# Kernel tuning notes

Measured on AMD Instinct MI355X. Metric: run time of the kernel, lower is better.

Reference implementation:

```python
import jax, jax.numpy as jnp
import numpy as np
from jax import lax

H = 16          # num heads
D_CONV = 4      # causal conv kernel width
NORMALIZER = 16.0
EPS = 1e-5


def _causal_conv_silu(x, w):
    # x: [B, L, D], w: [D, W] depthwise causal conv, then silu
    B, L, D = x.shape
    xp = jnp.pad(x, ((0, 0), (D_CONV - 1, 0), (0, 0)))
    y = sum(xp[:, k:k + L, :] * w[:, k] for k in range(D_CONV))
    return jax.nn.silu(y)


def _gla_scan(q, k, v, gk):
    # q,k,gk: [B,H,L,dk]; v: [B,H,L,dv]
    B, h, L, dk = q.shape
    dv = v.shape[-1]
    qT = jnp.moveaxis(q, 2, 0)
    kT = jnp.moveaxis(k, 2, 0)
    vT = jnp.moveaxis(v, 2, 0)
    gT = jnp.moveaxis(gk, 2, 0)

    def step(S, inp):
        qt, kt, vt, gt = inp  # [B,H,dk] / [B,H,dv]
        S = S * jnp.exp(gt)[..., None] + kt[..., None] * vt[..., None, :]
        ot = jnp.einsum('bhk,bhkv->bhv', qt, S)
        return S, ot

    S0 = jnp.zeros((B, h, dk, dv), q.dtype)
    S, o = lax.scan(step, S0, (qT, kT, vT, gT))
    return jnp.moveaxis(o, 0, 2), S  # [B,H,L,dv], final state


def setup_inputs() -> dict:
    key = jax.random.key(0)
    ks = jax.random.split(key, 9)
    L, B, D = 8192, 8, 1024
    s = lambda fan: 1.0 / np.sqrt(fan)
    return {
        'x': jax.random.normal(ks[0], (L, B, D), jnp.float32),
        'conv_w': jax.random.normal(ks[1], (D, D_CONV), jnp.float32) * s(D_CONV),
        'Wq': jax.random.normal(ks[2], (D, D // 2), jnp.float32) * s(D),
        'Wkg': jax.random.normal(ks[3], (D, D // 2), jnp.float32) * s(D),
        'Wv': jax.random.normal(ks[4], (D, D), jnp.float32) * s(D),
        'Wg': jax.random.normal(ks[5], (D, D), jnp.float32) * s(D),
        'bg': jax.random.normal(ks[6], (D,), jnp.float32) * 0.02,
        'Wout': jax.random.normal(ks[7], (D, D), jnp.float32) * s(D),
        'aug_balance': jnp.zeros((D // 2,), jnp.float32),
    }


def reference(x, conv_w, Wq, Wkg, Wv, Wg, bg, Wout, aug_balance):
    # x: [L, B, D] -> [B, L, D]
    xb = jnp.swapaxes(x, 0, 1)
    xb = _causal_conv_silu(xb, conv_w)

    q = xb @ Wq                      # [B,L,D/2]
    k_gate = xb @ Wkg                # [B,L,D/2]
    v = xb @ Wv                      # [B,L,D]
    g = xb @ Wg + bg                 # [B,L,D]

    gk = jax.nn.log_sigmoid(k_gate) / NORMALIZER
    k = 1.0 - jnp.exp(gk)

    B, L, _ = q.shape
    split = lambda t: t.reshape(B, L, H, -1).transpose(0, 2, 1, 3)  # b h l d
    qh, kh, gkh, vh = split(q), split(k), split(gk), split(v)
    dk = qh.shape[-1]

    # fused_chunk_gla default scale = dk ** -0.5 (applied to q internally)
    o, new_state = _gla_scan(qh * (dk ** -0.5), kh, vh, gkh)

    # meta self-augmentation (uses unscaled q)
    aug = aug_balance.reshape(H, dk)
    aug_w = jnp.einsum('bhlk,hk,bhlk->bhl', qh, aug, kh)
    o = o + jax.nn.sigmoid(aug_w[..., None] * vh)

    # group norm: LayerNorm over head_dim, no affine
    mu = o.mean(-1, keepdims=True)
    var = o.var(-1, keepdims=True)
    o = (o - mu) * lax.rsqrt(var + EPS)

    o = o.transpose(0, 2, 1, 3).reshape(B, L, -1)  # [B,L,D]
    out = (jax.nn.silu(g) * o) @ Wout
    return jnp.swapaxes(out, 0, 1), new_state  # [L,B,D], [B,H,dk,dv]
```

## Files before the change

### kernel.cpp

```cpp
#include <hip/hip_runtime.h>
#include <stdint.h>

typedef __attribute__((ext_vector_type(4))) float f32x4;
typedef _Float16 f16x8 __attribute__((ext_vector_type(8)));
typedef __attribute__((ext_vector_type(8))) unsigned short u16x8;
typedef __attribute__((ext_vector_type(2))) unsigned int u32x2;
typedef unsigned short u16;
typedef unsigned int u32;

#define LSEQ 8192
#define BB 8
#define DD 1024
#define MM 65536
#define NCH 128

__device__ __forceinline__ u16 f2h(float f) {
    _Float16 h = (_Float16)f;
    return *(u16*)&h;
}
__device__ __forceinline__ float h2f(u16 u) {
    _Float16 h = *(_Float16*)&u;
    return (float)h;
}

__device__ __forceinline__ void gload_lds16(const void* g, void* l) {
    __builtin_amdgcn_global_load_lds(
        (const __attribute__((address_space(1))) u32*)g,
        (__attribute__((address_space(3))) u32*)l, 16, 0, 0);
}

__global__ __launch_bounds__(256) void k_conv_silu(const float* __restrict__ x,
                                                   const float* __restrict__ w,
                                                   u16* __restrict__ xb) {
    int m = blockIdx.x;
    int b = m >> 13, l = m & 8191;
    int d0 = threadIdx.x * 4;
    f32x4 wv[4];
#pragma unroll
    for (int j = 0; j < 4; j++) wv[j] = *(const f32x4*)&w[(d0 + j) * 4];
    float acc[4] = {0.f, 0.f, 0.f, 0.f};
#pragma unroll
    for (int kk = 0; kk < 4; kk++) {
        int lp = l - 3 + kk;
        if (lp >= 0) {
            f32x4 xv = *(const f32x4*)&x[((size_t)(lp * BB + b)) * DD + d0];
#pragma unroll
            for (int j = 0; j < 4; j++) acc[j] += xv[j] * wv[j][kk];
        }
    }
    u16 o[4];
#pragma unroll
    for (int j = 0; j < 4; j++) {
        float a = acc[j];
        o[j] = f2h(a / (1.f + __expf(-a)));
    }
    u32x2 pk;
    pk.x = (u32)o[0] | ((u32)o[1] << 16);
    pk.y = (u32)o[2] | ((u32)o[3] << 16);
    *(u32x2*)&xb[(size_t)m * DD + d0] = pk;
}

__global__ __launch_bounds__(256) void k_packW(const float* __restrict__ Wq,
                                               const float* __restrict__ Wkg,
                                               const float* __restrict__ Wv,
                                               const float* __restrict__ Wg,
                                               const float* __restrict__ Wout,
                                               u16* __restrict__ Wcat,
                                               u16* __restrict__ WoutT) {
    int idx = blockIdx.x * 256 + threadIdx.x;
    const int T1 = 3072 * 1024;
    if (idx < T1) {
        int n = idx >> 10, kk = idx & 1023;
        float v;
        if (n < 512)        v = Wq [kk * 512 + n];
        else if (n < 1024)  v = Wkg[kk * 512 + (n - 512)];
        else if (n < 2048)  v = Wv [kk * 1024 + (n - 1024)];
        else                v = Wg [kk * 1024 + (n - 2048)];
        Wcat[idx] = f2h(v);
    } else {
        int j = idx - T1;
        if (j < 1024 * 1024) {
            int n = j >> 10, kk = j & 1023;
            WoutT[j] = f2h(Wout[kk * 1024 + n]);
        }
    }
}

template <int MODE>
__device__ __forceinline__ void epi_frag(f32x4 v, int grow0, int gcol,
                                         u16* __restrict__ qo, u16* __restrict__ gko,
                                         u16* __restrict__ ko, u16* __restrict__ vo,
                                         u16* __restrict__ sgo, const float* __restrict__ bg,
                                         float* __restrict__ out) {
#pragma unroll
    for (int rr = 0; rr < 4; rr++) {
        int grow = grow0 + rr;
        float val = v[rr];
        if (MODE == 1) {
            if (gcol < 512) {
                qo[(size_t)grow * 512 + gcol] = f2h(val);
            } else if (gcol < 1024) {
                float ls = fminf(val, 0.f) - log1pf(__expf(-fabsf(val)));
                float gkv = ls * 0.0625f;
                gko[(size_t)grow * 512 + (gcol - 512)] = f2h(gkv);
                ko [(size_t)grow * 512 + (gcol - 512)] = f2h(-expm1f(gkv));
            } else if (gcol < 2048) {
                vo[(size_t)grow * 1024 + (gcol - 1024)] = f2h(val);
            } else {
                float gg = val + bg[gcol - 2048];
                sgo[(size_t)grow * 1024 + (gcol - 2048)] = f2h(gg / (1.f + __expf(-gg)));
            }
        } else {
            int l = grow & 8191, b = grow >> 13;
            out[((size_t)(l * BB + b)) * DD + gcol] = val;
        }
    }
}

template <int MODE>
__global__ __launch_bounds__(256, 3) void k_gemm_bt(
    const u16* __restrict__ A, const u16* __restrict__ Bt, int nt_tiles,
    u16* __restrict__ qo, u16* __restrict__ gko, u16* __restrict__ ko,
    u16* __restrict__ vo, u16* __restrict__ sgo, const float* __restrict__ bg,
    float* __restrict__ out) {
    const int K = 1024;
    __shared__ __align__(16) u16 Sm[20480];
    int tid = threadIdx.x;
    int w = tid >> 6, lane = tid & 63;
    int wm = w >> 1, wn = w & 1;
    int lr = lane & 15, lk = lane >> 4;

    int xcd = blockIdx.x & 7;
    int cidx = blockIdx.x >> 3;
    int grpsz = nt_tiles * 4;
    int grp = cidx / grpsz;
    int r = cidx - grp * grpsz;
    int ntile = r >> 2;
    int mts_per_chunk = (gridDim.x >> 3) / nt_tiles;
    int mtile = xcd * mts_per_chunk + grp * 4 + (r & 3);
    int m0 = mtile << 8, n0 = ntile << 6;

#define DECL_ACC(MT) f32x4 a##MT##_0 = {0.f,0.f,0.f,0.f}, a##MT##_1 = {0.f,0.f,0.f,0.f};
    DECL_ACC(0) DECL_ACC(1) DECL_ACC(2) DECL_ACC(3)
    DECL_ACC(4) DECL_ACC(5) DECL_ACC(6) DECL_ACC(7)
#undef DECL_ACC

    int row = tid >> 2;
    int sslot = (tid & 3) ^ ((tid >> 3) & 3);
    const u16* gA = A + (size_t)(m0 + row) * K + sslot * 8;
    const u16* gB = Bt + (size_t)(n0 + row) * K + sslot * 8;
    char* lA = (char*)Sm + w * 1024;
    char* lB = (char*)Sm + 16384 + w * 1024;

#define STAGE(TT, OB) { \
    int k1 = (TT) << 5; \
    gload_lds16(gA + k1, lA + (OB)); \
    gload_lds16(gA + (size_t)64 * K + k1, lA + (OB) + 4096); \
    gload_lds16(gA + (size_t)128 * K + k1, lA + (OB) + 8192); \
    gload_lds16(gA + (size_t)192 * K + k1, lA + (OB) + 12288); \
    gload_lds16(gB + k1, lB + (OB)); }

#define MFMA_ROW(MT) { \
    f16x8 av = *(const f16x8*)&As[(wm * 128 + MT * 16 + lr) * 32 + acsl]; \
    a##MT##_0 = __builtin_amdgcn_mfma_f32_16x16x32_f16(av, b0, a##MT##_0, 0, 0, 0); \
    a##MT##_1 = __builtin_amdgcn_mfma_f32_16x16x32_f16(av, b1, a##MT##_1, 0, 0, 0); }

#define COMPUTE() { \
    int acsl = (lk ^ ((lr >> 1) & 3)) * 8; \
    f16x8 b0 = *(const f16x8*)&Bs[(wn * 32 +  0 + lr) * 32 + acsl]; \
    f16x8 b1 = *(const f16x8*)&Bs[(wn * 32 + 16 + lr) * 32 + acsl]; \
    __builtin_amdgcn_s_setprio(1); \
    MFMA_ROW(0) MFMA_ROW(1) MFMA_ROW(2) MFMA_ROW(3) \
    MFMA_ROW(4) MFMA_ROW(5) MFMA_ROW(6) MFMA_ROW(7) \
    __builtin_amdgcn_s_setprio(0); }

    STAGE(0, 0)
    STAGE(1, 20480)

    for (int t = 0; t < 31; ++t) {
        asm volatile("s_waitcnt vmcnt(5)" ::: "memory");
        __builtin_amdgcn_sched_barrier(0);
        __builtin_amdgcn_s_barrier();
        {
            const u16* As = Sm + (t & 1) * 10240;
            const u16* Bs = As + 8192;
            COMPUTE()
        }
        __builtin_amdgcn_s_barrier();
        __builtin_amdgcn_sched_barrier(0);
        if (t < 30) {
            STAGE(t + 2, (t & 1) * 20480)
        }
    }
    asm volatile("s_waitcnt vmcnt(0)" ::: "memory");
    __builtin_amdgcn_sched_barrier(0);
    __builtin_amdgcn_s_barrier();
    {
        const u16* As = Sm + 10240;
        const u16* Bs = As + 8192;
        COMPUTE()
    }
#undef COMPUTE
#undef MFMA_ROW
#undef STAGE

#define EPI_ROW(MT) { \
    int gr0 = m0 + wm * 128 + MT * 16 + lk * 4; \
    epi_frag<MODE>(a##MT##_0, gr0, n0 + wn * 32 +  0 + lr, qo, gko, ko, vo, sgo, bg, out); \
    epi_frag<MODE>(a##MT##_1, gr0, n0 + wn * 32 + 16 + lr, qo, gko, ko, vo, sgo, bg, out); }
    EPI_ROW(0) EPI_ROW(1) EPI_ROW(2) EPI_ROW(3)
    EPI_ROW(4) EPI_ROW(5) EPI_ROW(6) EPI_ROW(7)
#undef EPI_ROW
}

__global__ __launch_bounds__(64) void k_pass1(const u16* __restrict__ gkb,
                                              const u16* __restrict__ kb,
                                              const u16* __restrict__ vb,
                                              float* __restrict__ Mo,
                                              float* __restrict__ eGC) {
    __shared__ __align__(16) float kkT[64 * 32];
    int bhc = blockIdx.x;
    int c = bhc & 127, bh = bhc >> 7;
    int h = bh & 15, b = bh >> 4;
    int m0 = b * LSEQ + c * 64;
    int lane = threadIdx.x;
    if (lane < 32) {
        int i = lane;
        size_t base = (size_t)m0 * 512 + h * 32 + i;
        float G = 0.f;
        for (int t = 0; t < 64; t++) {
            G += h2f(gkb[base + (size_t)t * 512]);
            G = fmaxf(G, -60.f);
            kkT[t * 32 + i] = h2f(kb[base + (size_t)t * 512]) * __expf(-G);
        }
        eGC[bhc * 32 + i] = __expf(G);
    }
    __syncthreads();
    float Ma[32];
#pragma unroll
    for (int i = 0; i < 32; i++) Ma[i] = 0.f;
    size_t vbase = (size_t)m0 * 1024 + h * 64 + lane;
    for (int t = 0; t < 64; t++) {
        float vj = h2f(vb[vbase + (size_t)t * 1024]);
#pragma unroll
        for (int i4 = 0; i4 < 32; i4 += 4) {
            f32x4 kk4 = *(const f32x4*)&kkT[t * 32 + i4];
            Ma[i4 + 0] += kk4[0] * vj;
            Ma[i4 + 1] += kk4[1] * vj;
            Ma[i4 + 2] += kk4[2] * vj;
            Ma[i4 + 3] += kk4[3] * vj;
        }
    }
    size_t mb = (size_t)bhc * 2048 + lane;
#pragma unroll
    for (int i = 0; i < 32; i++) Mo[mb + i * 64] = Ma[i];
}

__global__ __launch_bounds__(64) void k_pass2(float* Mbuf, float* Sbuf,
                                              const float* __restrict__ eGC,
                                              float* __restrict__ state_out, int aliased) {
    int blk = blockIdx.x;
    int bh = blk >> 2, iq = blk & 3;
    int i0 = iq * 8;
    int j = threadIdx.x;
    float S[8];
#pragma unroll
    for (int i = 0; i < 8; i++) S[i] = 0.f;
    for (int c = 0; c < NCH; c++) {
        size_t base = ((size_t)bh * NCH + c) * 2048;
        float mv[8], ev[8];
#pragma unroll
        for (int i = 0; i < 8; i++) mv[i] = Mbuf[base + (i0 + i) * 64 + j];
#pragma unroll
        for (int i = 0; i < 8; i++) ev[i] = eGC[(bh * NCH + c) * 32 + i0 + i];
        if (aliased) { asm volatile("s_waitcnt vmcnt(0)" ::: "memory"); }
#pragma unroll
        for (int i = 0; i < 8; i++) Sbuf[base + (i0 + i) * 64 + j] = S[i];
#pragma unroll
        for (int i = 0; i < 8; i++) S[i] = (S[i] + mv[i]) * ev[i];
    }
    size_t so = (size_t)bh * 2048 + j;
#pragma unroll
    for (int i = 0; i < 8; i++) state_out[so + (i0 + i) * 64] = S[i];
}

__global__ __launch_bounds__(64) void k_pass3(const u16* __restrict__ qb,
                                              const u16* __restrict__ gkb,
                                              const u16* __restrict__ kb,
                                              const u16* __restrict__ vb,
                                              const u16* __restrict__ sgb,
                                              const float* __restrict__ Sbuf,
                                              const float* __restrict__ aug,
                                              u16* __restrict__ PRE) {
    __shared__ __align__(16) u16 qqT[64 * 32];
    __shared__ __align__(16) u16 kkT[64 * 32];
    __shared__ float awl[64];
    int bhc = blockIdx.x;
    int c = bhc & 127, bh = bhc >> 7;
    int h = bh & 15, b = bh >> 4;
    int m0 = b * LSEQ + c * 64;
    int lane = threadIdx.x;
    const float scale = 0.17677669529663689f;
    if (lane < 32) {
        int i = lane;
        size_t base = (size_t)m0 * 512 + h * 32 + i;
        float G = 0.f;
        for (int t = 0; t < 64; t++) {
            float gkv = h2f(gkb[base + (size_t)t * 512]);
            float qv  = h2f(qb [base + (size_t)t * 512]);
            float kv  = h2f(kb [base + (size_t)t * 512]);
            G += gkv;
            G = fmaxf(G, -60.f);
            qqT[t * 32 + i] = f2h(qv * __expf(G) * scale);
            kkT[t * 32 + i] = f2h(kv * __expf(-G));
        }
    }
    {
        int i = lane & 31;
        int th = (lane >> 5) << 5;
        float augi = aug[h * 32 + i];
        size_t base2 = (size_t)m0 * 512 + h * 32 + i;
        for (int tt = 0; tt < 32; tt++) {
            int t = tt + th;
            float qv = h2f(qb[base2 + (size_t)t * 512]);
            float kv = h2f(kb[base2 + (size_t)t * 512]);
            float p = qv * kv * augi;
            p += __shfl_xor(p, 1);
            p += __shfl_xor(p, 2);
            p += __shfl_xor(p, 4);
            p += __shfl_xor(p, 8);
            p += __shfl_xor(p, 16);
            if (i == 0) awl[t] = p;
        }
    }
    __syncthreads();
    float T[32];
    size_t sb = (size_t)bhc * 2048 + lane;
#pragma unroll
    for (int i = 0; i < 32; i++) T[i] = Sbuf[sb + i * 64];
    size_t vbase = (size_t)m0 * 1024 + h * 64 + lane;
    for (int t = 0; t < 64; t++) {
        float vj  = h2f(vb [vbase + (size_t)t * 1024]);
        float sgj = h2f(sgb[vbase + (size_t)t * 1024]);
        float aw = awl[t];
        float o0 = 0.f, o1 = 0.f, o2 = 0.f, o3 = 0.f;
        u16x8 kk8a = *(const u16x8*)&kkT[t * 32 + 0];
        u16x8 qq8a = *(const u16x8*)&qqT[t * 32 + 0];
        u16x8 kk8b = *(const u16x8*)&kkT[t * 32 + 8];
        u16x8 qq8b = *(const u16x8*)&qqT[t * 32 + 8];
        u16x8 kk8c = *(const u16x8*)&kkT[t * 32 + 16];
        u16x8 qq8c = *(const u16x8*)&qqT[t * 32 + 16];
        u16x8 kk8d = *(const u16x8*)&kkT[t * 32 + 24];
        u16x8 qq8d = *(const u16x8*)&qqT[t * 32 + 24];
#pragma unroll
        for (int e = 0; e < 8; e++) {
            T[e]      += h2f(kk8a[e]) * vj;  o0 += h2f(qq8a[e]) * T[e];
            T[8 + e]  += h2f(kk8b[e]) * vj;  o1 += h2f(qq8b[e]) * T[8 + e];
            T[16 + e] += h2f(kk8c[e]) * vj;  o2 += h2f(qq8c[e]) * T[16 + e];
            T[24 + e] += h2f(kk8d[e]) * vj;  o3 += h2f(qq8d[e]) * T[24 + e];
        }
        float o = (o0 + o1) + (o2 + o3);
        o += 1.f / (1.f + __expf(-aw * vj));
        float s1 = o, s2 = o * o;
#pragma unroll
        for (int msk = 1; msk < 64; msk <<= 1) {
            s1 += __shfl_xor(s1, msk);
            s2 += __shfl_xor(s2, msk);
        }
        float mu = s1 * 0.015625f;
        float var = s2 * 0.015625f - mu * mu;
        float on = (o - mu) * rsqrtf(fmaxf(var, 0.f) + 1e-5f);
        PRE[vbase + (size_t)t * 1024] = f2h(on * sgj);
    }
}

extern "C" void kernel_launch(void* const* d_in, const int* in_sizes, int n_in,
                              void* d_out, int out_size, void* d_ws, size_t ws_size,
                              hipStream_t stream) {
    (void)in_sizes; (void)n_in; (void)out_size;
    const float* x      = (const float*)d_in[0];
    const float* conv_w = (const float*)d_in[1];
    const float* Wq     = (const float*)d_in[2];
    const float* Wkg    = (const float*)d_in[3];
    const float* Wv     = (const float*)d_in[4];
    const float* Wg     = (const float*)d_in[5];
    const float* bg     = (const float*)d_in[6];
    const float* Wout   = (const float*)d_in[7];
    const float* aug    = (const float*)d_in[8];

    char* ws = (char*)d_ws;
    u16*   xb    = (u16*)  (ws + 0);
    u16*   Wcat  = (u16*)  (ws + 134217728);
    u16*   WoutT = (u16*)  (ws + 140509184);
    u16*   qb    = (u16*)  (ws + 142606336);
    u16*   gkb   = (u16*)  (ws + 209715200);
    u16*   kbuf  = (u16*)  (ws + 276824064);
    u16*   sgb   = (u16*)  (ws + 343932928);
    float* Mbuf  = (float*)(ws + 478150656);
    float* eGC   = (float*)(ws + 612368384);
    float* Sb    = (float*)(ws + 614465536);
    const size_t REQ_FULL = 748683264ull;
    int aliased = (ws_size < REQ_FULL) ? 1 : 0;
    float* Sbuf = aliased ? Mbuf : Sb;

    float* out = (float*)d_out;
    float* state_out = out + 67108864;
    u16* vb = (u16*)d_out;

    k_conv_silu<<<dim3(65536), dim3(256), 0, stream>>>(x, conv_w, xb);
    k_packW<<<dim3(16384), dim3(256), 0, stream>>>(Wq, Wkg, Wv, Wg, Wout, Wcat, WoutT);
    k_gemm_bt<1><<<dim3(12288), dim3(256), 0, stream>>>(xb, Wcat, 48,
                                                        qb, gkb, kbuf, vb, sgb, bg, nullptr);
    k_pass1<<<dim3(16384), dim3(64), 0, stream>>>(gkb, kbuf, vb, Mbuf, eGC);
    k_pass2<<<dim3(512), dim3(64), 0, stream>>>(Mbuf, Sbuf, eGC, state_out, aliased);
    k_pass3<<<dim3(16384), dim3(64), 0, stream>>>(qb, gkb, kbuf, vb, sgb, Sbuf, aug, xb );
    k_gemm_bt<2><<<dim3(4096), dim3(256), 0, stream>>>(xb, WoutT, 16,
                                                       nullptr, nullptr, nullptr, nullptr, nullptr, nullptr, out);
}
```

Baseline: 1.696 ms.

## Split pass3 intra-chunk recurrence across four waves with prefix state sums

```diff
diff --git a/kernel.cpp b/kernel.cpp
--- a/kernel.cpp
+++ b/kernel.cpp
@@ -284,24 +284,26 @@
     for (int i = 0; i < 8; i++) state_out[so + (i0 + i) * 64] = S[i];
 }
 
-__global__ __launch_bounds__(64) void k_pass3(const u16* __restrict__ qb,
-                                              const u16* __restrict__ gkb,
-                                              const u16* __restrict__ kb,
-                                              const u16* __restrict__ vb,
-                                              const u16* __restrict__ sgb,
-                                              const float* __restrict__ Sbuf,
-                                              const float* __restrict__ aug,
-                                              u16* __restrict__ PRE) {
+__global__ __launch_bounds__(256) void k_pass3(const u16* __restrict__ qb,
+                                               const u16* __restrict__ gkb,
+                                               const u16* __restrict__ kb,
+                                               const u16* __restrict__ vb,
+                                               const u16* __restrict__ sgb,
+                                               const float* __restrict__ Sbuf,
+                                               const float* __restrict__ aug,
+                                               u16* __restrict__ PRE) {
     __shared__ __align__(16) u16 qqT[64 * 32];
     __shared__ __align__(16) u16 kkT[64 * 32];
     __shared__ float awl[64];
+    __shared__ __align__(16) float Qbuf[3][32][64];
     int bhc = blockIdx.x;
     int c = bhc & 127, bh = bhc >> 7;
     int h = bh & 15, b = bh >> 4;
     int m0 = b * LSEQ + c * 64;
-    int lane = threadIdx.x;
+    int tid = threadIdx.x;
+    int wv = tid >> 6, lane = tid & 63;
     const float scale = 0.17677669529663689f;
-    if (lane < 32) {
+    if (wv == 0 && lane < 32) {
         int i = lane;
         size_t base = (size_t)m0 * 512 + h * 32 + i;
         float G = 0.f;
@@ -315,12 +317,13 @@
             kkT[t * 32 + i] = f2h(kv * __expf(-G));
         }
     }
-    {
+    if (wv == 1 || wv == 2) {
         int i = lane & 31;
         int th = (lane >> 5) << 5;
         float augi = aug[h * 32 + i];
         size_t base2 = (size_t)m0 * 512 + h * 32 + i;
-        for (int tt = 0; tt < 32; tt++) {
+        int tt0 = (wv - 1) * 16;
+        for (int tt = tt0; tt < tt0 + 16; tt++) {
             int t = tt + th;
             float qv = h2f(qb[base2 + (size_t)t * 512]);
             float kv = h2f(kb[base2 + (size_t)t * 512]);
@@ -334,12 +337,40 @@
         }
     }
     __syncthreads();
+    size_t vbase = (size_t)m0 * 1024 + h * 64 + lane;
+    if (wv >= 1) {
+        int s0 = (wv - 1) * 16;
+        float Q[32];
+#pragma unroll
+        for (int i = 0; i < 32; i++) Q[i] = 0.f;
+        for (int s = s0; s < s0 + 16; s++) {
+            float vj = h2f(vb[vbase + (size_t)s * 1024]);
+            u16x8 k8a = *(const u16x8*)&kkT[s * 32 + 0];
+            u16x8 k8b = *(const u16x8*)&kkT[s * 32 + 8];
+            u16x8 k8c = *(const u16x8*)&kkT[s * 32 + 16];
+            u16x8 k8d = *(const u16x8*)&kkT[s * 32 + 24];
+#pragma unroll
+            for (int e = 0; e < 8; e++) {
+                Q[e]      += h2f(k8a[e]) * vj;
+                Q[8 + e]  += h2f(k8b[e]) * vj;
+                Q[16 + e] += h2f(k8c[e]) * vj;
+                Q[24 + e] += h2f(k8d[e]) * vj;
+            }
+        }
+#pragma unroll
+        for (int i = 0; i < 32; i++) Qbuf[wv - 1][i][lane] = Q[i];
+    }
+    __syncthreads();
     float T[32];
     size_t sb = (size_t)bhc * 2048 + lane;
 #pragma unroll
     for (int i = 0; i < 32; i++) T[i] = Sbuf[sb + i * 64];
-    size_t vbase = (size_t)m0 * 1024 + h * 64 + lane;
-    for (int t = 0; t < 64; t++) {
+    for (int w2 = 0; w2 < wv; w2++) {
+#pragma unroll
+        for (int i = 0; i < 32; i++) T[i] += Qbuf[w2][i][lane];
+    }
+    int t0 = wv * 16;
+    for (int t = t0; t < t0 + 16; t++) {
         float vj  = h2f(vb [vbase + (size_t)t * 1024]);
         float sgj = h2f(sgb[vbase + (size_t)t * 1024]);
         float aw = awl[t];
@@ -413,7 +444,7 @@
                                                         qb, gkb, kbuf, vb, sgb, bg, nullptr);
     k_pass1<<<dim3(16384), dim3(64), 0, stream>>>(gkb, kbuf, vb, Mbuf, eGC);
     k_pass2<<<dim3(512), dim3(64), 0, stream>>>(Mbuf, Sbuf, eGC, state_out, aliased);
-    k_pass3<<<dim3(16384), dim3(64), 0, stream>>>(qb, gkb, kbuf, vb, sgb, Sbuf, aug, xb );
+    k_pass3<<<dim3(16384), dim3(256), 0, stream>>>(qb, gkb, kbuf, vb, sgb, Sbuf, aug, xb );
     k_gemm_bt<2><<<dim3(4096), dim3(256), 0, stream>>>(xb, WoutT, 16,
                                                        nullptr, nullptr, nullptr, nullptr, nullptr, nullptr, out);
 }
```

Measured after the change: 1.873 ms. 1.1x slower.
